# Performance work log

Hardware: AMD Instinct MI355X
Metric: run time of the kernel (lower is better)

Reference implementation:

```python
import jax, jax.numpy as jnp
import numpy as np

EPS = 1e-12  # F.normalize default eps

def setup_inputs() -> dict:
    key = jax.random.key(0)
    ks = jax.random.split(key, 8)
    nq, lq, nd, ld, H, E = 64, 32, 256, 180, 768, 128
    return {
        "query_hidden": jax.random.normal(ks[0], (nq, lq, H), jnp.float32),
        "doc_hidden": jax.random.normal(ks[1], (nd, ld, H), jnp.float32),
        "query_mask": jax.random.randint(ks[2], (nq, lq), 0, 2, jnp.int32).at[:, 0].set(1),
        "doc_punct_mask": jax.random.randint(ks[3], (nd, ld), 0, 2, jnp.int32).at[:, 0].set(1),
        "W1": jax.random.normal(ks[4], (H, H), jnp.float32) * (1.0 / np.sqrt(H)),
        "b1": jnp.zeros((H,), jnp.float32),
        "W2": jax.random.normal(ks[5], (H, E), jnp.float32) * (1.0 / np.sqrt(H)),
        "b2": jnp.zeros((E,), jnp.float32),
    }

def _head(h, W1, b1, W2, b2):
    # embedding_head: Linear -> ReLU -> (Dropout, eval) -> Linear
    return jax.nn.relu(h @ W1 + b1) @ W2 + b2

def _l2norm(x):
    n = jnp.linalg.norm(x, axis=-1, keepdims=True)
    return x / jnp.maximum(n, EPS)

def reference(query_hidden, doc_hidden, query_mask, doc_punct_mask, W1, b1, W2, b2):
    qm = query_mask.astype(jnp.float32)          # [nq, lq]
    dm = doc_punct_mask.astype(jnp.float32)      # [nd, ld]
    # query(): project, mask, L2-normalize per token
    qe = _l2norm(_head(query_hidden, W1, b1, W2, b2) * qm[..., None])  # [nq, lq, E]
    # doc(): project, punctuation-mask, L2-normalize per token
    de = _l2norm(_head(doc_hidden, W1, b1, W2, b2) * dm[..., None])    # [nd, ld, E]
    # score_cart: full cartesian MaxSim
    scores = jnp.einsum('qih,djh->qidj', qe, de)  # [nq, lq, nd, ld]
    masked = scores * dm[None, None, :, :]
    # max over doc tokens, sum over query tokens, normalize by query length
    s = masked.max(axis=-1).sum(axis=1) / qm.sum(axis=-1, keepdims=True)  # [nq, nd]
    return s
```

## Files before the change

kernel.cpp:

```cpp
#include <hip/hip_runtime.h>
#include <hip/hip_bf16.h>

#define H_DIM 768
#define E_DIM 128
#define NQ 64
#define LQ 32
#define ND 256
#define LD 180
#define QTOK (NQ*LQ)
#define DTOK (ND*LD)
#define TTOK (QTOK+DTOK)

typedef __attribute__((ext_vector_type(8))) short short8;
typedef __attribute__((ext_vector_type(4))) float f32x4;
typedef __attribute__((ext_vector_type(4))) float float4v;

__device__ __forceinline__ unsigned short f2bf(float f) {
    union { float f; unsigned u; } v;
    v.f = f;
    unsigned r = v.u + 0x7fffu + ((v.u >> 16) & 1u);
    return (unsigned short)(r >> 16);
}

__device__ __forceinline__ void gl_lds16(const void* g, void* l) {
    __builtin_amdgcn_global_load_lds(
        (const __attribute__((address_space(1))) unsigned char*)g,
        (__attribute__((address_space(3))) unsigned char*)l, 16, 0, 0);
}

__global__ __launch_bounds__(256) void prep_kernel(
    const float* __restrict__ W1, const float* __restrict__ W2,
    const int* __restrict__ qmask,
    unsigned short* __restrict__ W1T, unsigned short* __restrict__ W2T,
    float* __restrict__ qcnt)
{
    int tid = blockIdx.x * 256 + threadIdx.x;
    int nth = gridDim.x * 256;
    for (int idx = tid; idx < H_DIM * H_DIM; idx += nth) {
        int k = idx / H_DIM, c = idx - k * H_DIM;
        W1T[(size_t)c * H_DIM + k] = f2bf(W1[idx]);
    }
    for (int idx = tid; idx < H_DIM * E_DIM; idx += nth) {
        int k = idx / E_DIM, c = idx - k * E_DIM;
        W2T[(size_t)c * H_DIM + k] = f2bf(W2[idx]);
    }
    if (tid < NQ) {
        int s = 0;
        for (int i = 0; i < LQ; ++i) s += qmask[tid * LQ + i];
        qcnt[tid] = (float)s;
    }
}

__global__ __launch_bounds__(256, 3) void head_kernel(
    const float* __restrict__ qh, const float* __restrict__ dh,
    const int* __restrict__ qmv, const int* __restrict__ dmv,
    const float* __restrict__ b1, const float* __restrict__ b2,
    const unsigned short* __restrict__ W1T, const unsigned short* __restrict__ W2T,
    unsigned short* __restrict__ emb, unsigned short* __restrict__ xbf)
{
    __shared__ char lds[40960];
    char* Abuf = lds;
    char* Bbuf = lds + 8192;
    char* T1   = lds + 24576;

    const int tid = threadIdx.x;
    const int lane = tid & 63;
    const int wv = tid >> 6;
    const int wm = wv >> 1, wn = wv & 1;
    const int l15 = lane & 15, lhi = lane >> 4;
    const int t0 = blockIdx.x * 64;

    const float* xsrc = (t0 < QTOK) ? (qh + (size_t)t0 * H_DIM)
                                    : (dh + (size_t)(t0 - QTOK) * H_DIM);
    const int srow = tid >> 2;
    const int sseg = tid & 3;

    int bcol[4], bk[4];
    #pragma unroll
    for (int i = 0; i < 4; ++i) {
        int o = i * 4096 + wv * 1024 + lane * 16;
        int col = o >> 7;
        int kk = ((o & 127) ^ ((col & 7) << 4)) >> 1;
        bcol[i] = col; bk[i] = kk;
    }

    const f32x4 zero4 = {0.f, 0.f, 0.f, 0.f};
    f32x4 eacc[2][4];
    #pragma unroll
    for (int mt = 0; mt < 2; ++mt)
        #pragma unroll
        for (int nt = 0; nt < 4; ++nt) eacc[mt][nt] = zero4;

    for (int jb = 0; jb < 6; ++jb) {
        f32x4 pacc[2][4];
        #pragma unroll
        for (int mt = 0; mt < 2; ++mt)
            #pragma unroll
            for (int nt = 0; nt < 4; ++nt) pacc[mt][nt] = zero4;

        for (int kb = 0; kb < 12; ++kb) {
            __syncthreads();
            #pragma unroll
            for (int i = 0; i < 4; ++i)
                gl_lds16(W1T + (size_t)(jb * 128 + bcol[i]) * H_DIM + kb * 64 + bk[i],
                         Bbuf + i * 4096 + wv * 1024);

            short8 afx[2][2];
            if (jb == 0) {
                const float* s = xsrc + (size_t)srow * H_DIM + kb * 64 + sseg * 16;
                union { unsigned short u[16]; short8 s8[2]; } t16;
                #pragma unroll
                for (int i = 0; i < 4; ++i) {
                    float4v v = *(const float4v*)(s + i * 4);
                    t16.u[i*4+0] = f2bf(v.x); t16.u[i*4+1] = f2bf(v.y);
                    t16.u[i*4+2] = f2bf(v.z); t16.u[i*4+3] = f2bf(v.w);
                }
                int base = srow * 128 + sseg * 32;
                int sw = (srow & 7) << 4;
                *(short8*)(Abuf + (base ^ sw)) = t16.s8[0];
                *(short8*)(Abuf + ((base + 16) ^ sw)) = t16.s8[1];
                if (xbf) {
                    unsigned short* xd = xbf + (size_t)(t0 + srow) * H_DIM + kb * 64 + sseg * 16;
                    *(short8*)(xd) = t16.s8[0];
                    *(short8*)(xd + 8) = t16.s8[1];
                }
            } else if (xbf) {
                #pragma unroll
                for (int mt = 0; mt < 2; ++mt)
                    #pragma unroll
                    for (int ks = 0; ks < 2; ++ks)
                        afx[mt][ks] = *(const short8*)(xbf +
                            (size_t)(t0 + wm*32 + mt*16 + l15) * H_DIM + kb*64 + ks*32 + lhi*8);
            } else {
                #pragma unroll
                for (int mt = 0; mt < 2; ++mt)
                    #pragma unroll
                    for (int ks = 0; ks < 2; ++ks) {
                        const float* p = xsrc + (size_t)(wm*32 + mt*16 + l15) * H_DIM + kb*64 + ks*32 + lhi*8;
                        float4v a = ((const float4v*)p)[0], b = ((const float4v*)p)[1];
                        union { unsigned short u[8]; short8 s8; } tt;
                        tt.u[0]=f2bf(a.x); tt.u[1]=f2bf(a.y); tt.u[2]=f2bf(a.z); tt.u[3]=f2bf(a.w);
                        tt.u[4]=f2bf(b.x); tt.u[5]=f2bf(b.y); tt.u[6]=f2bf(b.z); tt.u[7]=f2bf(b.w);
                        afx[mt][ks] = tt.s8;
                    }
            }
            __syncthreads();
            if (jb == 0) {
                #pragma unroll
                for (int mt = 0; mt < 2; ++mt)
                    #pragma unroll
                    for (int ks = 0; ks < 2; ++ks) {
                        int row = wm*32 + mt*16 + l15;
                        int byte = (row * 128 + (ks*32 + lhi*8) * 2) ^ ((row & 7) << 4);
                        afx[mt][ks] = *(const short8*)(Abuf + byte);
                    }
            }
            #pragma unroll
            for (int ks = 0; ks < 2; ++ks) {
                short8 bfr[4];
                #pragma unroll
                for (int nt = 0; nt < 4; ++nt) {
                    int col = wn*64 + nt*16 + l15;
                    int byte = (col * 128 + (ks*32 + lhi*8) * 2) ^ ((col & 7) << 4);
                    bfr[nt] = *(const short8*)(Bbuf + byte);
                }
                #pragma unroll
                for (int nt = 0; nt < 4; ++nt)
                    #pragma unroll
                    for (int mt = 0; mt < 2; ++mt)
                        pacc[mt][nt] = __builtin_amdgcn_mfma_f32_16x16x32_bf16(
                            bfr[nt], afx[mt][ks], pacc[mt][nt], 0, 0, 0);
            }
        }

        #pragma unroll
        for (int mt = 0; mt < 2; ++mt) {
            int token = wm*32 + mt*16 + l15;
            int sw = (token & 7) << 4;
            #pragma unroll
            for (int nt = 0; nt < 4; ++nt) {
                int c0 = wn*64 + nt*16 + lhi*4;
                union { unsigned short u[4]; unsigned long long q; } pk;
                #pragma unroll
                for (int r = 0; r < 4; ++r) {
                    float v = pacc[mt][nt][r] + b1[jb*128 + c0 + r];
                    v = v > 0.f ? v : 0.f;
                    pk.u[r] = f2bf(v);
                }
                int byte = (token * 256 + c0 * 2) ^ sw;
                *(unsigned long long*)(T1 + byte) = pk.q;
            }
        }

        #pragma unroll
        for (int h = 0; h < 2; ++h) {
            __syncthreads();
            #pragma unroll
            for (int i = 0; i < 4; ++i)
                gl_lds16(W2T + (size_t)bcol[i] * H_DIM + jb * 128 + h * 64 + bk[i],
                         Bbuf + i * 4096 + wv * 1024);
            __syncthreads();
            #pragma unroll
            for (int ks = 0; ks < 2; ++ks) {
                short8 at[2], bw[4];
                #pragma unroll
                for (int mt = 0; mt < 2; ++mt) {
                    int row = wm*32 + mt*16 + l15;
                    int byte = (row * 256 + (h*64 + ks*32 + lhi*8) * 2) ^ ((row & 7) << 4);
                    at[mt] = *(const short8*)(T1 + byte);
                }
                #pragma unroll
                for (int nt = 0; nt < 4; ++nt) {
                    int col = wn*64 + nt*16 + l15;
                    int byte = (col * 128 + (ks*32 + lhi*8) * 2) ^ ((col & 7) << 4);
                    bw[nt] = *(const short8*)(Bbuf + byte);
                }
                #pragma unroll
                for (int mt = 0; mt < 2; ++mt)
                    #pragma unroll
                    for (int nt = 0; nt < 4; ++nt)
                        eacc[mt][nt] = __builtin_amdgcn_mfma_f32_16x16x32_bf16(
                            at[mt], bw[nt], eacc[mt][nt], 0, 0, 0);
            }
        }
    }

    float* rs = (float*)lds;
    float b2v[4];
    #pragma unroll
    for (int nt = 0; nt < 4; ++nt) b2v[nt] = b2[wn*64 + nt*16 + l15];

    float vals[2][4][4], sq[2][4];
    #pragma unroll
    for (int mt = 0; mt < 2; ++mt)
        #pragma unroll
        for (int r = 0; r < 4; ++r) {
            int ri = mt*16 + lhi*4 + r;
            int t = t0 + wm*32 + ri;
            float fm = (float)((t < QTOK) ? qmv[t] : dmv[t - QTOK]);
            float s = 0.f;
            #pragma unroll
            for (int nt = 0; nt < 4; ++nt) {
                float v = (eacc[mt][nt][r] + b2v[nt]) * fm;
                vals[mt][nt][r] = v;
                s += v * v;
            }
            sq[mt][r] = s;
        }
    #pragma unroll
    for (int m1 = 1; m1 < 16; m1 <<= 1)
        #pragma unroll
        for (int mt = 0; mt < 2; ++mt)
            #pragma unroll
            for (int r = 0; r < 4; ++r)
                sq[mt][r] += __shfl_xor(sq[mt][r], m1, 64);
    __syncthreads();
    if (l15 == 0) {
        #pragma unroll
        for (int mt = 0; mt < 2; ++mt)
            #pragma unroll
            for (int r = 0; r < 4; ++r)
                rs[wv*32 + mt*16 + lhi*4 + r] = sq[mt][r];
    }
    __syncthreads();
    #pragma unroll
    for (int mt = 0; mt < 2; ++mt)
        #pragma unroll
        for (int r = 0; r < 4; ++r) {
            int ri = mt*16 + lhi*4 + r;
            float tot = rs[(wm*2)*32 + ri] + rs[(wm*2+1)*32 + ri];
            float sc = 1.f / fmaxf(sqrtf(tot), 1e-12f);
            int t = t0 + wm*32 + ri;
            #pragma unroll
            for (int nt = 0; nt < 4; ++nt)
                emb[(size_t)t * E_DIM + wn*64 + nt*16 + l15] = f2bf(vals[mt][nt][r] * sc);
        }
}

__global__ __launch_bounds__(256, 3) void score_kernel(
    const unsigned short* __restrict__ emb, const int* __restrict__ dmask,
    const float* __restrict__ qcnt, float* __restrict__ out)
{
    __shared__ char slds[16384 + 64];
    char* De = slds;
    float* red = (float*)(slds + 16384);

    const int d = blockIdx.x & 255;
    const int qg = blockIdx.x >> 8;
    const int tid = threadIdx.x, lane = tid & 63, wv = tid >> 6;
    const int l15 = lane & 15, lhi = lane >> 4;
    const int srow = tid >> 2, sseg = tid & 3;

    short8 af[4][4];
    #pragma unroll
    for (int mt = 0; mt < 4; ++mt)
        #pragma unroll
        for (int ks = 0; ks < 4; ++ks)
            af[mt][ks] = *(const short8*)(emb +
                (size_t)(qg*256 + wv*64 + mt*16 + l15) * E_DIM + ks*32 + lhi*8);

    float rmax[4][4];
    #pragma unroll
    for (int mt = 0; mt < 4; ++mt)
        #pragma unroll
        for (int r = 0; r < 4; ++r) rmax[mt][r] = -3.0e38f;

    const f32x4 zero4 = {0.f, 0.f, 0.f, 0.f};
    for (int ch = 0; ch < 3; ++ch) {
        int j = ch*64 + srow;
        int jv = (j < LD) ? j : 0;
        const unsigned short* src = emb + (size_t)(QTOK + d*LD + jv) * E_DIM + sseg*32;
        if (ch) __syncthreads();
        #pragma unroll
        for (int i = 0; i < 4; ++i) {
            short8 v = *(const short8*)(src + i*8);
            int byte = (srow * 256 + (sseg*32 + i*8) * 2) ^ ((srow & 7) << 4);
            *(short8*)(De + byte) = v;
        }
        __syncthreads();
        #pragma unroll
        for (int nt = 0; nt < 4; ++nt) {
            short8 bfr[4];
            int col = nt*16 + l15;
            #pragma unroll
            for (int ks = 0; ks < 4; ++ks) {
                int byte = (col * 256 + (ks*32 + lhi*8) * 2) ^ ((col & 7) << 4);
                bfr[ks] = *(const short8*)(De + byte);
            }
            f32x4 acc[4] = {zero4, zero4, zero4, zero4};
            #pragma unroll
            for (int ks = 0; ks < 4; ++ks)
                #pragma unroll
                for (int mt = 0; mt < 4; ++mt)
                    acc[mt] = __builtin_amdgcn_mfma_f32_16x16x32_bf16(
                        af[mt][ks], bfr[ks], acc[mt], 0, 0, 0);
            int jcol = ch*64 + nt*16 + l15;
            float mval = (jcol < LD) ? (float)dmask[d*LD + jcol] : -1.f;
            #pragma unroll
            for (int mt = 0; mt < 4; ++mt)
                #pragma unroll
                for (int r = 0; r < 4; ++r) {
                    float v = (mval < 0.f) ? -3.0e38f : acc[mt][r] * mval;
                    rmax[mt][r] = fmaxf(rmax[mt][r], v);
                }
        }
    }
    #pragma unroll
    for (int m1 = 1; m1 < 16; m1 <<= 1)
        #pragma unroll
        for (int mt = 0; mt < 4; ++mt)
            #pragma unroll
            for (int r = 0; r < 4; ++r)
                rmax[mt][r] = fmaxf(rmax[mt][r], __shfl_xor(rmax[mt][r], m1, 64));
    float s0 = 0.f, s1 = 0.f;
    #pragma unroll
    for (int r = 0; r < 4; ++r) { s0 += rmax[0][r] + rmax[1][r]; s1 += rmax[2][r] + rmax[3][r]; }
    s0 += __shfl_xor(s0, 16, 64); s0 += __shfl_xor(s0, 32, 64);
    s1 += __shfl_xor(s1, 16, 64); s1 += __shfl_xor(s1, 32, 64);
    if (lane == 0) { red[wv*2 + 0] = s0; red[wv*2 + 1] = s1; }
    __syncthreads();
    if (tid < 8) {
        int q = qg*8 + tid;
        out[q * ND + d] = red[tid] / qcnt[q];
    }
}

extern "C" void kernel_launch(void* const* d_in, const int* in_sizes, int n_in,
                              void* d_out, int out_size, void* d_ws, size_t ws_size,
                              hipStream_t stream)
{
    const float* qh = (const float*)d_in[0];
    const float* dh = (const float*)d_in[1];
    const int*   qm = (const int*)d_in[2];
    const int*   dm = (const int*)d_in[3];
    const float* W1 = (const float*)d_in[4];
    const float* b1 = (const float*)d_in[5];
    const float* W2 = (const float*)d_in[6];
    const float* b2 = (const float*)d_in[7];
    float* out = (float*)d_out;

    unsigned short* emb = (unsigned short*)d_ws;
    unsigned short* W1T = emb + (size_t)TTOK * E_DIM;
    unsigned short* W2T = W1T + (size_t)H_DIM * H_DIM;
    float* qcnt = (float*)(W2T + (size_t)E_DIM * H_DIM);
    size_t base_need = (size_t)TTOK*E_DIM*2 + (size_t)H_DIM*H_DIM*2
                     + (size_t)E_DIM*H_DIM*2 + 256;
    size_t xbf_need = (size_t)TTOK * H_DIM * 2;
    unsigned short* xbf = nullptr;
    if (ws_size >= base_need + xbf_need)
        xbf = (unsigned short*)((char*)d_ws + base_need);

    prep_kernel<<<256, 256, 0, stream>>>(W1, W2, qm, W1T, W2T, qcnt);
    head_kernel<<<TTOK / 64, 256, 0, stream>>>(qh, dh, qm, dm, b1, b2, W1T, W2T, emb, xbf);
    score_kernel<<<8 * ND, 256, 0, stream>>>(emb, dm, qcnt, out);
}
```

Before: 243.6 us.

## Pre-convert activations to MFMA fragment-packed bf16 in prep kernel

Moves the fp32-to-bf16 conversion of all hidden states out of the head kernel's first jb pass into the prep kernel. It writes them in a layout where each wave's A fragment is a contiguous 1KB block, so the head kernel reads fragments with coalesced loads and no longer needs the LDS A buffer. LDS per block drops and launch bounds rise to 4 blocks per CU, and the weight transpose is rewritten to make output writes coalesced. In exchange, the prep kernel becomes a full extra pass over the input and grows to a larger grid.

```diff
diff --git a/kernel.cpp b/kernel.cpp
--- a/kernel.cpp
+++ b/kernel.cpp
@@ -29,60 +29,91 @@
 }
 
 __global__ __launch_bounds__(256) void prep_kernel(
+    const float* __restrict__ qh, const float* __restrict__ dh,
     const float* __restrict__ W1, const float* __restrict__ W2,
     const int* __restrict__ qmask,
     unsigned short* __restrict__ W1T, unsigned short* __restrict__ W2T,
-    float* __restrict__ qcnt)
+    float* __restrict__ qcnt, unsigned short* __restrict__ xbf2)
 {
     int tid = blockIdx.x * 256 + threadIdx.x;
     int nth = gridDim.x * 256;
-    for (int idx = tid; idx < H_DIM * H_DIM; idx += nth) {
-        int k = idx / H_DIM, c = idx - k * H_DIM;
-        W1T[(size_t)c * H_DIM + k] = f2bf(W1[idx]);
-    }
-    for (int idx = tid; idx < H_DIM * E_DIM; idx += nth) {
-        int k = idx / E_DIM, c = idx - k * E_DIM;
-        W2T[(size_t)c * H_DIM + k] = f2bf(W2[idx]);
+    for (int o = tid; o < H_DIM * H_DIM; o += nth) {
+        int c = o / H_DIM, k = o - c * H_DIM;
+        W1T[o] = f2bf(W1[(size_t)k * H_DIM + c]);
+    }
+    for (int o = tid; o < E_DIM * H_DIM; o += nth) {
+        int c = o / H_DIM, k = o - c * H_DIM;
+        W2T[o] = f2bf(W2[(size_t)k * E_DIM + c]);
     }
     if (tid < NQ) {
         int s = 0;
         for (int i = 0; i < LQ; ++i) s += qmask[tid * LQ + i];
         qcnt[tid] = (float)s;
     }
-}
-
-__global__ __launch_bounds__(256, 3) void head_kernel(
+    if (xbf2) {
+        const int NSLOT = (TTOK / 16) * 12 * 128;
+        for (int S = tid; S < NSLOT; S += nth) {
+            int sic = S & 127;
+            int chunk = S >> 7;
+            int kb = chunk % 12;
+            int g  = chunk / 12;
+            int ks  = sic >> 6;
+            int lh2 = (sic >> 4) & 3;
+            int L   = sic & 15;
+            int row = g * 16 + L;
+            int k0  = kb * 64 + ks * 32 + lh2 * 8;
+            const float* src = (row < QTOK)
+                ? (qh + (size_t)row * H_DIM + k0)
+                : (dh + (size_t)(row - QTOK) * H_DIM + k0);
+            float4v a = ((const float4v*)src)[0];
+            float4v b = ((const float4v*)src)[1];
+            union { unsigned short u[8]; short8 s8; } t;
+            t.u[0] = f2bf(a.x); t.u[1] = f2bf(a.y); t.u[2] = f2bf(a.z); t.u[3] = f2bf(a.w);
+            t.u[4] = f2bf(b.x); t.u[5] = f2bf(b.y); t.u[6] = f2bf(b.z); t.u[7] = f2bf(b.w);
+            *(short8*)(xbf2 + (size_t)S * 8) = t.s8;
+        }
+    }
+}
+
+__global__ __launch_bounds__(256, 4) void head_kernel(
     const float* __restrict__ qh, const float* __restrict__ dh,
     const int* __restrict__ qmv, const int* __restrict__ dmv,
     const float* __restrict__ b1, const float* __restrict__ b2,
     const unsigned short* __restrict__ W1T, const unsigned short* __restrict__ W2T,
-    unsigned short* __restrict__ emb, unsigned short* __restrict__ xbf)
+    unsigned short* __restrict__ emb, const unsigned short* __restrict__ xbf2)
 {
-    __shared__ char lds[40960];
-    char* Abuf = lds;
-    char* Bbuf = lds + 8192;
-    char* T1   = lds + 24576;
-
-    const int tid = threadIdx.x;
-    const int lane = tid & 63;
-    const int wv = tid >> 6;
+    __shared__ char lds[32768];
+    char* Bbuf = lds;
+    char* T1   = lds + 16384;
+
+    const int tid = threadIdx.x, lane = tid & 63, wv = tid >> 6;
     const int wm = wv >> 1, wn = wv & 1;
     const int l15 = lane & 15, lhi = lane >> 4;
     const int t0 = blockIdx.x * 64;
-
     const float* xsrc = (t0 < QTOK) ? (qh + (size_t)t0 * H_DIM)
                                     : (dh + (size_t)(t0 - QTOK) * H_DIM);
-    const int srow = tid >> 2;
-    const int sseg = tid & 3;
 
     int bcol[4], bk[4];
     #pragma unroll
     for (int i = 0; i < 4; ++i) {
         int o = i * 4096 + wv * 1024 + lane * 16;
         int col = o >> 7;
-        int kk = ((o & 127) ^ ((col & 7) << 4)) >> 1;
-        bcol[i] = col; bk[i] = kk;
-    }
+        bcol[i] = col;
+        bk[i] = ((o & 127) ^ ((col & 7) << 4)) >> 1;
+    }
+
+    #define STAGE_W1(JB, KB) do {                                              \
+        _Pragma("unroll")                                                      \
+        for (int i_ = 0; i_ < 4; ++i_)                                         \
+            gl_lds16(W1T + (size_t)((JB)*128 + bcol[i_]) * H_DIM + (KB)*64 + bk[i_], \
+                     Bbuf + i_*4096 + wv*1024);                                \
+    } while (0)
+    #define STAGE_W2(JB, HH) do {                                              \
+        _Pragma("unroll")                                                      \
+        for (int i_ = 0; i_ < 4; ++i_)                                         \
+            gl_lds16(W2T + (size_t)bcol[i_] * H_DIM + (JB)*128 + (HH)*64 + bk[i_], \
+                     Bbuf + i_*4096 + wv*1024);                                \
+    } while (0)
 
     const f32x4 zero4 = {0.f, 0.f, 0.f, 0.f};
     f32x4 eacc[2][4];
@@ -91,6 +122,7 @@
         #pragma unroll
         for (int nt = 0; nt < 4; ++nt) eacc[mt][nt] = zero4;
 
+    #pragma unroll 1
     for (int jb = 0; jb < 6; ++jb) {
         f32x4 pacc[2][4];
         #pragma unroll
@@ -98,39 +130,21 @@
             #pragma unroll
             for (int nt = 0; nt < 4; ++nt) pacc[mt][nt] = zero4;
 
+        #pragma unroll 1
         for (int kb = 0; kb < 12; ++kb) {
             __syncthreads();
-            #pragma unroll
-            for (int i = 0; i < 4; ++i)
-                gl_lds16(W1T + (size_t)(jb * 128 + bcol[i]) * H_DIM + kb * 64 + bk[i],
-                         Bbuf + i * 4096 + wv * 1024);
+            STAGE_W1(jb, kb);
 
             short8 afx[2][2];
-            if (jb == 0) {
-                const float* s = xsrc + (size_t)srow * H_DIM + kb * 64 + sseg * 16;
-                union { unsigned short u[16]; short8 s8[2]; } t16;
-                #pragma unroll
-                for (int i = 0; i < 4; ++i) {
-                    float4v v = *(const float4v*)(s + i * 4);
-                    t16.u[i*4+0] = f2bf(v.x); t16.u[i*4+1] = f2bf(v.y);
-                    t16.u[i*4+2] = f2bf(v.z); t16.u[i*4+3] = f2bf(v.w);
-                }
-                int base = srow * 128 + sseg * 32;
-                int sw = (srow & 7) << 4;
-                *(short8*)(Abuf + (base ^ sw)) = t16.s8[0];
-                *(short8*)(Abuf + ((base + 16) ^ sw)) = t16.s8[1];
-                if (xbf) {
-                    unsigned short* xd = xbf + (size_t)(t0 + srow) * H_DIM + kb * 64 + sseg * 16;
-                    *(short8*)(xd) = t16.s8[0];
-                    *(short8*)(xd + 8) = t16.s8[1];
-                }
-            } else if (xbf) {
+            if (xbf2) {
                 #pragma unroll
                 for (int mt = 0; mt < 2; ++mt)
                     #pragma unroll
-                    for (int ks = 0; ks < 2; ++ks)
-                        afx[mt][ks] = *(const short8*)(xbf +
-                            (size_t)(t0 + wm*32 + mt*16 + l15) * H_DIM + kb*64 + ks*32 + lhi*8);
+                    for (int ks = 0; ks < 2; ++ks) {
+                        size_t r16 = (size_t)(t0 >> 4) + wm * 2 + mt;
+                        afx[mt][ks] = *(const short8*)(xbf2 +
+                            ((r16 * 12 + kb) * 2 + ks) * 512 + lhi * 128 + l15 * 8);
+                    }
             } else {
                 #pragma unroll
                 for (int mt = 0; mt < 2; ++mt)
@@ -145,23 +159,14 @@
                     }
             }
             __syncthreads();
-            if (jb == 0) {
-                #pragma unroll
-                for (int mt = 0; mt < 2; ++mt)
-                    #pragma unroll
-                    for (int ks = 0; ks < 2; ++ks) {
-                        int row = wm*32 + mt*16 + l15;
-                        int byte = (row * 128 + (ks*32 + lhi*8) * 2) ^ ((row & 7) << 4);
-                        afx[mt][ks] = *(const short8*)(Abuf + byte);
-                    }
-            }
+
             #pragma unroll
             for (int ks = 0; ks < 2; ++ks) {
                 short8 bfr[4];
                 #pragma unroll
                 for (int nt = 0; nt < 4; ++nt) {
-                    int col = wn*64 + nt*16 + l15;
-                    int byte = (col * 128 + (ks*32 + lhi*8) * 2) ^ ((col & 7) << 4);
+                    int col = wn * 64 + nt * 16 + l15;
+                    int byte = (col * 128 + (ks * 32 + lhi * 8) * 2) ^ ((col & 7) << 4);
                     bfr[nt] = *(const short8*)(Bbuf + byte);
                 }
                 #pragma unroll
@@ -175,15 +180,15 @@
 
         #pragma unroll
         for (int mt = 0; mt < 2; ++mt) {
-            int token = wm*32 + mt*16 + l15;
+            int token = wm * 32 + mt * 16 + l15;
             int sw = (token & 7) << 4;
             #pragma unroll
             for (int nt = 0; nt < 4; ++nt) {
-                int c0 = wn*64 + nt*16 + lhi*4;
+                int c0 = wn * 64 + nt * 16 + lhi * 4;
                 union { unsigned short u[4]; unsigned long long q; } pk;
                 #pragma unroll
                 for (int r = 0; r < 4; ++r) {
-                    float v = pacc[mt][nt][r] + b1[jb*128 + c0 + r];
+                    float v = pacc[mt][nt][r] + b1[jb * 128 + c0 + r];
                     v = v > 0.f ? v : 0.f;
                     pk.u[r] = f2bf(v);
                 }
@@ -192,27 +197,24 @@
             }
         }
 
-        #pragma unroll
+        #pragma unroll 1
         for (int h = 0; h < 2; ++h) {
             __syncthreads();
-            #pragma unroll
-            for (int i = 0; i < 4; ++i)
-                gl_lds16(W2T + (size_t)bcol[i] * H_DIM + jb * 128 + h * 64 + bk[i],
-                         Bbuf + i * 4096 + wv * 1024);
+            STAGE_W2(jb, h);
             __syncthreads();
             #pragma unroll
             for (int ks = 0; ks < 2; ++ks) {
                 short8 at[2], bw[4];
                 #pragma unroll
                 for (int mt = 0; mt < 2; ++mt) {
-                    int row = wm*32 + mt*16 + l15;
-                    int byte = (row * 256 + (h*64 + ks*32 + lhi*8) * 2) ^ ((row & 7) << 4);
+                    int row = wm * 32 + mt * 16 + l15;
+                    int byte = (row * 256 + (h * 64 + ks * 32 + lhi * 8) * 2) ^ ((row & 7) << 4);
                     at[mt] = *(const short8*)(T1 + byte);
                 }
                 #pragma unroll
                 for (int nt = 0; nt < 4; ++nt) {
-                    int col = wn*64 + nt*16 + l15;
-                    int byte = (col * 128 + (ks*32 + lhi*8) * 2) ^ ((col & 7) << 4);
+                    int col = wn * 64 + nt * 16 + l15;
+                    int byte = (col * 128 + (ks * 32 + lhi * 8) * 2) ^ ((col & 7) << 4);
                     bw[nt] = *(const short8*)(Bbuf + byte);
                 }
                 #pragma unroll
@@ -275,6 +277,8 @@
             for (int nt = 0; nt < 4; ++nt)
                 emb[(size_t)t * E_DIM + wn*64 + nt*16 + l15] = f2bf(vals[mt][nt][r] * sc);
         }
+    #undef STAGE_W1
+    #undef STAGE_W2
 }
 
 __global__ __launch_bounds__(256, 3) void score_kernel(
@@ -386,11 +390,11 @@
     size_t base_need = (size_t)TTOK*E_DIM*2 + (size_t)H_DIM*H_DIM*2
                      + (size_t)E_DIM*H_DIM*2 + 256;
     size_t xbf_need = (size_t)TTOK * H_DIM * 2;
-    unsigned short* xbf = nullptr;
+    unsigned short* xbf2 = nullptr;
     if (ws_size >= base_need + xbf_need)
-        xbf = (unsigned short*)((char*)d_ws + base_need);
-
-    prep_kernel<<<256, 256, 0, stream>>>(W1, W2, qm, W1T, W2T, qcnt);
-    head_kernel<<<TTOK / 64, 256, 0, stream>>>(qh, dh, qm, dm, b1, b2, W1T, W2T, emb, xbf);
+        xbf2 = (unsigned short*)((char*)d_ws + base_need);
+
+    prep_kernel<<<2048, 256, 0, stream>>>(qh, dh, W1, W2, qm, W1T, W2T, qcnt, xbf2);
+    head_kernel<<<TTOK / 64, 256, 0, stream>>>(qh, dh, qm, dm, b1, b2, W1T, W2T, emb, xbf2);
     score_kernel<<<8 * ND, 256, 0, stream>>>(emb, dm, qcnt, out);
 }
```

Result: faster. 217.0 us (-10.9%).
